# Kernel tuning notes

Hardware: AMD Instinct MI355X
Metric: run time of the kernel (lower is better)

The kernel has to match this reference:

```python
import jax, jax.numpy as jnp
import numpy as np

# Module config (from init_kwargs)
B = 1024          # batch
CIN = 1024        # in_channels
COUT = 2048       # out_channels
K = 7             # kernel_size; input spatial must equal K so deform-conv out is 1x1
STRIDE, PAD, DIL, DG = 1, 0, 1, 1  # stride, padding, dilation, deformable_groups
H = W = K


def setup_inputs() -> dict:
    key = jax.random.key(0)
    k1, k2, k3, k4, k5, k6 = jax.random.split(key, 6)
    x = jax.random.normal(k1, (B, CIN, H, W), dtype=jnp.float32)
    # offset-predicting conv: Conv2d(CIN, 2*K*K*DG, K, bias=False); small init so offsets are a few pixels
    offset_w = jax.random.normal(k2, (2 * DG * K * K, CIN, K, K), dtype=jnp.float32) * 0.01
    # deformable conv weight/bias (kaiming-like scale)
    deform_w = jax.random.normal(k3, (COUT, CIN, K, K), dtype=jnp.float32) * (1.0 / np.sqrt(CIN * K * K))
    deform_b = jax.random.normal(k4, (COUT,), dtype=jnp.float32) * 0.01
    # fused linear COUT -> COUT
    lin_w = jax.random.normal(k5, (COUT, COUT), dtype=jnp.float32) * (1.0 / np.sqrt(COUT))
    lin_b = jax.random.normal(k6, (COUT,), dtype=jnp.float32) * 0.01
    return {"x": x, "offset_w": offset_w, "deform_w": deform_w,
            "deform_b": deform_b, "lin_w": lin_w, "lin_b": lin_b}


def _deform_conv2d(x, offset, weight, bias):
    """torchvision deform_conv2d (v1, no modulation mask), groups=1.
    x: [B, C, H, W]; offset: [B, 2*DG*K*K, Ho, Wo] ordered (dg, kh, kw, (dy,dx)).
    """
    Bn, C, Hx, Wx = x.shape
    Cout, _, Kh, Kw = weight.shape
    P = Kh * Kw
    Ho, Wo = offset.shape[2], offset.shape[3]
    L = Ho * Wo
    Cg = C // DG

    off = offset.reshape(Bn, DG, P, 2, Ho, Wo)
    ky = jnp.repeat(jnp.arange(Kh), Kw).astype(x.dtype)   # [P]
    kx = jnp.tile(jnp.arange(Kw), Kh).astype(x.dtype)     # [P]
    base_y = (jnp.arange(Ho) * STRIDE - PAD).astype(x.dtype)  # [Ho]
    base_x = (jnp.arange(Wo) * STRIDE - PAD).astype(x.dtype)  # [Wo]
    # sampling positions [B, DG, P, Ho, Wo]
    py = off[:, :, :, 0] + (ky * DIL)[None, None, :, None, None] + base_y[None, None, None, :, None]
    px = off[:, :, :, 1] + (kx * DIL)[None, None, :, None, None] + base_x[None, None, None, None, :]

    y0 = jnp.floor(py); x0 = jnp.floor(px)
    fy = py - y0;       fx = px - x0
    y0i = y0.astype(jnp.int32); x0i = x0.astype(jnp.int32)

    xg = x.reshape(Bn, DG, Cg, Hx * Wx)
    acc = jnp.zeros((Bn, DG, Cg, P * L), x.dtype)
    for di, wy in ((0, 1.0 - fy), (1, fy)):
        for dj, wx in ((0, 1.0 - fx), (1, fx)):
            yi = y0i + di
            xi = x0i + dj
            valid = (yi >= 0) & (yi < Hx) & (xi >= 0) & (xi < Wx)  # zero-pad outside
            idx = (jnp.clip(yi, 0, Hx - 1) * Wx + jnp.clip(xi, 0, Wx - 1)).reshape(Bn, DG, 1, P * L)
            wgt = (wy * wx * valid.astype(x.dtype)).reshape(Bn, DG, 1, P * L)
            g = jnp.take_along_axis(xg, jnp.broadcast_to(idx, (Bn, DG, Cg, P * L)), axis=-1)
            acc = acc + g * wgt
    # columns: [B, C*P, L] with (channel, kernel-tap) ordering matching weight layout
    cols = acc.reshape(Bn, DG, Cg, P, L).reshape(Bn, C * P, L)
    out = jnp.einsum('ok,bkl->bol', weight.reshape(Cout, C * P), cols) + bias[None, :, None]
    return out.reshape(Bn, Cout, Ho, Wo)


def reference(x, offset_w, deform_w, deform_b, lin_w, lin_b):
    # 1) offset-predicting conv (bias=False)
    offset = jax.lax.conv_general_dilated(
        x, offset_w, window_strides=(STRIDE, STRIDE),
        padding=[(PAD, PAD), (PAD, PAD)], rhs_dilation=(DIL, DIL),
        dimension_numbers=('NCHW', 'OIHW', 'NCHW'))  # [B, 2*DG*K*K, 1, 1]
    # 2) deformable conv
    y = _deform_conv2d(x, offset, deform_w, deform_b)  # [B, COUT, 1, 1]
    # 3) linear over flattened features (spatial is 1x1 so flat dim == COUT)
    y = y.reshape(B, COUT) @ lin_w.T + lin_b
    # 4) softshrink(lambd=0.5)
    y = jnp.where(y > 0.5, y - 0.5, jnp.where(y < -0.5, y + 0.5, jnp.zeros_like(y)))
    return y.reshape(B, COUT, 1, 1)
```

## Files before the change

### kernel.cpp

```cpp
#include <hip/hip_runtime.h>

typedef _Float16 f16;
typedef _Float16 f16x8 __attribute__((ext_vector_type(8)));
typedef float f32x4 __attribute__((ext_vector_type(4)));

#define DEVI static __device__ __forceinline__

DEVI void async_ld16(const void* g, void* l) {
  __builtin_amdgcn_global_load_lds(
      (const __attribute__((address_space(1))) unsigned int*)g,
      (__attribute__((address_space(3))) unsigned int*)l, 16, 0, 0);
}

DEVI int sw_off(int row, int q) {
  return row * 64 + ((q ^ ((row >> 1) & 3)) << 4);
}

template<bool A_F32>
__global__ __launch_bounds__(256, 4)
void gemm_bt(const void* __restrict__ Aptr, const f16* __restrict__ Bt,
             float* __restrict__ Cpart, int ldK, int Nvalid,
             int mTiles, int nTiles, int kPerSplit, int Mtot) {
  __shared__ __align__(16) f16 As[128 * 32];
  __shared__ __align__(16) f16 Bs[128 * 32];

  int nb = gridDim.x;
  int bid = (blockIdx.x & 7) * (nb >> 3) + (blockIdx.x >> 3);
  int ms = bid % mTiles; bid /= mTiles;
  int ns = bid % nTiles; bid /= nTiles;
  int ks = bid;
  int m0 = ms * 128, n0 = ns * 128;
  int k0 = ks * kPerSplit;

  int tid = threadIdx.x;
  int w = tid >> 6, lane = tid & 63;
  int wrow = (w >> 1) * 64, wcol = (w & 1) * 64;
  int lrow = lane & 15, lquad = lane >> 4;

  f32x4 acc[4][4];
#pragma unroll
  for (int i = 0; i < 4; ++i)
#pragma unroll
    for (int j = 0; j < 4; ++j) acc[i][j] = (f32x4){0.f, 0.f, 0.f, 0.f};

  for (int kk = k0; kk < k0 + kPerSplit; kk += 32) {
    __syncthreads();
#pragma unroll
    for (int s = 0; s < 2; ++s) {
      int rl = w * 32 + s * 16 + (lane >> 2);
      int qp = lane & 3;
      int q = qp ^ ((rl >> 1) & 3);
      int rb = n0 + rl; if (rb > Nvalid - 1) rb = Nvalid - 1;
      async_ld16(Bt + (size_t)rb * ldK + kk + q * 8, &Bs[(w * 32 + s * 16) * 32]);
    }
    if (!A_F32) {
      const f16* Ah = (const f16*)Aptr;
#pragma unroll
      for (int s = 0; s < 2; ++s) {
        int rl = w * 32 + s * 16 + (lane >> 2);
        int qp = lane & 3;
        int q = qp ^ ((rl >> 1) & 3);
        async_ld16(Ah + (size_t)(m0 + rl) * ldK + kk + q * 8, &As[(w * 32 + s * 16) * 32]);
      }
    } else {
      const float* Af = (const float*)Aptr;
      int r = tid >> 1, half = tid & 1;
      const float* src = Af + (size_t)(m0 + r) * ldK + kk + half * 16;
#pragma unroll
      for (int u2 = 0; u2 < 2; ++u2) {
        f32x4 a = *(const f32x4*)(src + u2 * 8);
        f32x4 b = *(const f32x4*)(src + u2 * 8 + 4);
        f16x8 h;
        h[0] = (f16)a[0]; h[1] = (f16)a[1]; h[2] = (f16)a[2]; h[3] = (f16)a[3];
        h[4] = (f16)b[0]; h[5] = (f16)b[1]; h[6] = (f16)b[2]; h[7] = (f16)b[3];
        *(f16x8*)((char*)As + sw_off(r, half * 2 + u2)) = h;
      }
    }
    __syncthreads();

    f16x8 af[4], bf[4];
#pragma unroll
    for (int i = 0; i < 4; ++i)
      af[i] = *(const f16x8*)((const char*)As + sw_off(wrow + i * 16 + lrow, lquad));
#pragma unroll
    for (int j = 0; j < 4; ++j)
      bf[j] = *(const f16x8*)((const char*)Bs + sw_off(wcol + j * 16 + lrow, lquad));
#pragma unroll
    for (int i = 0; i < 4; ++i)
#pragma unroll
      for (int j = 0; j < 4; ++j)
        acc[i][j] = __builtin_amdgcn_mfma_f32_16x16x32_f16(af[i], bf[j], acc[i][j], 0, 0, 0);
  }

  size_t base = (size_t)ks * Mtot * Nvalid;
#pragma unroll
  for (int i = 0; i < 4; ++i) {
    int row = m0 + wrow + i * 16 + lquad * 4;
#pragma unroll
    for (int j = 0; j < 4; ++j) {
      int col = n0 + wcol + j * 16 + lrow;
      if (col < Nvalid) {
#pragma unroll
        for (int r = 0; r < 4; ++r)
          Cpart[base + (size_t)(row + r) * Nvalid + col] = acc[i][j][r];
      }
    }
  }
}

__global__ void cvt_f32_to_f16(const float* __restrict__ in, f16* __restrict__ out, long n) {
  long idx = ((long)blockIdx.x * blockDim.x + threadIdx.x) * 8;
  if (idx + 8 <= n) {
    f32x4 a = *(const f32x4*)(in + idx);
    f32x4 b = *(const f32x4*)(in + idx + 4);
    f16x8 o;
    o[0] = (f16)a[0]; o[1] = (f16)a[1]; o[2] = (f16)a[2]; o[3] = (f16)a[3];
    o[4] = (f16)b[0]; o[5] = (f16)b[1]; o[6] = (f16)b[2]; o[7] = (f16)b[3];
    *(f16x8*)(out + idx) = o;
  }
}

__global__ __launch_bounds__(256, 4)
void build_cols(const float* __restrict__ x, const float* __restrict__ offs,
                f16* __restrict__ cols) {
  int b = blockIdx.x >> 3;
  int c0 = (blockIdx.x & 7) * 128;
  __shared__ __align__(16) float s_x[128 * 49];
  __shared__ __align__(16) int   s_idx[49][4];
  __shared__ __align__(16) float s_w[49][4];
  int t = threadIdx.x;
  if (t < 49) {
    float dy = offs[b * 98 + 2 * t];
    float dx = offs[b * 98 + 2 * t + 1];
    float py = dy + (float)(t / 7);
    float px = dx + (float)(t % 7);
    float fy0 = floorf(py), fx0 = floorf(px);
    int y0 = (int)fy0, x0 = (int)fx0;
    float fy = py - fy0, fx = px - fx0;
#pragma unroll
    for (int di = 0; di < 2; ++di)
#pragma unroll
      for (int dj = 0; dj < 2; ++dj) {
        int yi = y0 + di, xi = x0 + dj;
        bool valid = (yi >= 0) && (yi < 7) && (xi >= 0) && (xi < 7);
        int yc = yi < 0 ? 0 : (yi > 6 ? 6 : yi);
        int xc = xi < 0 ? 0 : (xi > 6 ? 6 : xi);
        float wy = di ? fy : 1.f - fy;
        float wx = dj ? fx : 1.f - fx;
        s_idx[t][di * 2 + dj] = yc * 7 + xc;
        s_w[t][di * 2 + dj] = valid ? wy * wx : 0.f;
      }
  }
  const f32x4* xs = (const f32x4*)(x + (size_t)b * 50176 + c0 * 49);
  f32x4* s4 = (f32x4*)s_x;
#pragma unroll
  for (int i = 0; i < 6; ++i) s4[t + i * 256] = xs[t + i * 256];
  if (t < 32) s4[1536 + t] = xs[1536 + t];
  __syncthreads();

  f16* cb = cols + (size_t)b * 50176 + c0 * 49;
#pragma unroll
  for (int i = 0; i < 25; ++i) {
    int o = t + i * 256;
    if (o < 6272) {
      unsigned c = (unsigned)o / 49u;
      unsigned p = (unsigned)o - c * 49u;
      int4  gi = *(const int4*)s_idx[p];
      float4 gw = *(const float4*)s_w[p];
      const float* row = s_x + c * 49;
      float v = gw.x * row[gi.x] + gw.y * row[gi.y]
              + gw.z * row[gi.z] + gw.w * row[gi.w];
      cb[o] = (f16)v;
    }
  }
}

__global__ void combine_k(const float* __restrict__ parts, int nparts, size_t pstride,
                          const float* __restrict__ bias, float* __restrict__ outf,
                          f16* __restrict__ outh, int total, int cols, int shrink) {
  int i = blockIdx.x * 256 + threadIdx.x;
  if (i >= total) return;
  float s = 0.f;
  for (int p = 0; p < nparts; ++p) s += parts[(size_t)p * pstride + i];
  if (bias) s += bias[i % cols];
  if (shrink) s = s > 0.5f ? s - 0.5f : (s < -0.5f ? s + 0.5f : 0.f);
  if (outf) outf[i] = s;
  if (outh) outh[i] = (f16)s;
}

extern "C" void kernel_launch(void* const* d_in, const int* in_sizes, int n_in,
                              void* d_out, int out_size, void* d_ws, size_t ws_size,
                              hipStream_t stream) {
  const float* x  = (const float*)d_in[0];
  const float* ow = (const float*)d_in[1];
  const float* dw = (const float*)d_in[2];
  const float* db = (const float*)d_in[3];
  const float* lw = (const float*)d_in[4];
  const float* lb = (const float*)d_in[5];
  float* out = (float*)d_out;

  const long KX = 50176;
  char* ws = (char*)d_ws;
  size_t off = 0;
  auto alloc = [&](size_t bytes) {
    char* p = ws + off;
    off = (off + bytes + 255) & ~(size_t)255;
    return p;
  };
  f16*   dw_h = (f16*)  alloc((size_t)2048 * KX * 2);
  f16*   ow_h = (f16*)  alloc((size_t)98 * KX * 2);
  f16*   lw_h = (f16*)  alloc((size_t)2048 * 2048 * 2);
  f16*   cols = (f16*)  alloc((size_t)1024 * KX * 2);
  float* y1p  = (float*)alloc((size_t)8 * 1024 * 2048 * 4);
  f16*   y1h  = (f16*)  alloc((size_t)1024 * 2048 * 2);
  float* offs = (float*)y1p;
  float* offp = (float*)((char*)y1p + (1u << 20));
  float* y2p  = (float*)cols;
  if (off > ws_size) return;

  long n_dw = 2048L * KX, n_ow = 98L * KX, n_lw = 2048L * 2048L;
  cvt_f32_to_f16<<<(unsigned)(n_dw / 8 / 256), 256, 0, stream>>>(dw, dw_h, n_dw);
  cvt_f32_to_f16<<<(unsigned)(n_ow / 8 / 256), 256, 0, stream>>>(ow, ow_h, n_ow);
  cvt_f32_to_f16<<<(unsigned)(n_lw / 8 / 256), 256, 0, stream>>>(lw, lw_h, n_lw);

  gemm_bt<true><<<8 * 1 * 98, 256, 0, stream>>>(
      x, ow_h, offp, 50176, 98, 8, 1, 512, 1024);
  combine_k<<<(1024 * 98 + 255) / 256, 256, 0, stream>>>(
      offp, 98, (size_t)1024 * 98, nullptr, offs, nullptr, 1024 * 98, 98, 0);

  build_cols<<<1024 * 8, 256, 0, stream>>>(x, offs, cols);

  gemm_bt<false><<<8 * 16 * 8, 256, 0, stream>>>(
      cols, dw_h, y1p, 50176, 2048, 8, 16, 6272, 1024);
  combine_k<<<(2097152 + 255) / 256, 256, 0, stream>>>(
      y1p, 8, (size_t)2097152, db, nullptr, y1h, 2097152, 2048, 0);

  gemm_bt<false><<<8 * 16 * 8, 256, 0, stream>>>(
      y1h, lw_h, y2p, 2048, 2048, 8, 16, 256, 1024);
  combine_k<<<(2097152 + 255) / 256, 256, 0, stream>>>(
      y2p, 8, (size_t)2097152, lb, out, nullptr, 2097152, 2048, 1);
}
```

Measured before the change: 1.115 ms.

## Replace main deform GEMM with 256x256 double-buffered pipelined MFMA kernel

Result: faster. 1.032 ms (-7.4%).

```diff
diff --git a/kernel.cpp b/kernel.cpp
--- a/kernel.cpp
+++ b/kernel.cpp
@@ -107,6 +107,133 @@
     }
   }
 }
+
+#define DSR(dst, addr, off) \
+  asm volatile("ds_read_b128 %0, %1 offset:" off : "=&v"(dst) : "v"(addr))
+
+#define PHASE(BUF, KK, RH, RDB, STG, VMF, VMS, BAR) do {                      \
+    unsigned aP = aAddr + (unsigned)((BUF)*32768 + (KK)*16384 + (RH)*4096);   \
+    DSR(af[0], aP, "0");    DSR(af[1], aP, "1024");                           \
+    DSR(af[2], aP, "2048"); DSR(af[3], aP, "3072");                           \
+    if (RDB) {                                                                \
+      unsigned bP = bAddr + (unsigned)((BUF)*32768 + (KK)*16384);             \
+      DSR(bf[0], bP, "0");    DSR(bf[1], bP, "1024");                         \
+      DSR(bf[2], bP, "2048"); DSR(bf[3], bP, "3072");                         \
+    }                                                                         \
+    STG;                                                                      \
+    if (BAR) __builtin_amdgcn_s_barrier();                                    \
+    asm volatile("s_waitcnt lgkmcnt(0)");                                     \
+    __builtin_amdgcn_sched_barrier(0);                                        \
+    __builtin_amdgcn_s_setprio(1);                                            \
+    _Pragma("unroll")                                                         \
+    for (int i_ = 0; i_ < 4; ++i_) {                                          \
+      _Pragma("unroll")                                                       \
+      for (int j_ = 0; j_ < 4; ++j_)                                          \
+        acc[(RH)*4 + i_][j_] = __builtin_amdgcn_mfma_f32_16x16x32_f16(        \
+            af[i_], bf[j_], acc[(RH)*4 + i_][j_], 0, 0, 0);                   \
+    }                                                                         \
+    __builtin_amdgcn_s_setprio(0);                                            \
+    if (VMF) asm volatile("s_waitcnt vmcnt(" VMS ")");                        \
+    if (BAR) __builtin_amdgcn_s_barrier();                                    \
+  } while (0)
+
+__global__ __launch_bounds__(512, 2)
+void gemm256(const f16* __restrict__ A, const f16* __restrict__ Bt,
+             float* __restrict__ Cpart, int ldK,
+             int mTiles, int nTiles, int kPerSplit, int Mtot, int Ntot) {
+  __shared__ __align__(16) f16 lds[65536];
+
+  int nb = gridDim.x;
+  int bid = (blockIdx.x & 7) * (nb >> 3) + (blockIdx.x >> 3);
+  int ms = bid % mTiles; bid /= mTiles;
+  int ns = bid % nTiles; bid /= nTiles;
+  int ks = bid;
+  int m0 = ms * 256, n0 = ns * 256;
+  long k0 = (long)ks * kPerSplit;
+  int NT = kPerSplit >> 6;
+
+  int tid = threadIdx.x;
+  int w = tid >> 6, lane = tid & 63;
+  int wrow = (w >> 2) * 128, wcol = (w & 3) * 64;
+  int lrow = lane & 15;
+  unsigned sq = (unsigned)((((lane >> 4) ^ ((lrow >> 1) & 3))) << 4);
+
+  char* ldsc = (char*)&lds[0];
+  unsigned ldsBase = (unsigned)(uintptr_t)(void*)&lds[0];
+  unsigned aAddr = ldsBase + (unsigned)((wrow + lrow) * 64) + sq;
+  unsigned bAddr = ldsBase + 65536u + (unsigned)((wcol + lrow) * 64) + sq;
+
+  const f16* Ab = A + (size_t)m0 * ldK + k0;
+  const f16* Bb = Bt + (size_t)n0 * ldK + k0;
+  int rs = (w * 2) * 16 + (lane >> 2);
+  int qg = ((lane & 3) ^ ((rs >> 1) & 3)) * 8;
+  const f16* a0 = Ab + (size_t)rs * ldK + qg;
+  const f16* b0 = Bb + (size_t)rs * ldK + qg;
+  const f16* a1 = a0 + (size_t)16 * ldK;
+  const f16* b1 = b0 + (size_t)16 * ldK;
+
+#define STGP(p0, p1, LOFF, KOFF) do {                                \
+    async_ld16(p0 + (KOFF), ldsc + (LOFF) + (w * 2) * 1024);         \
+    async_ld16(p1 + (KOFF), ldsc + (LOFF) + (w * 2) * 1024 + 1024);  \
+  } while (0)
+#define STG_A(BUF, KK, KT) STGP(a0, a1, (BUF)*32768 + (KK)*16384, (KT)*64 + (KK)*32)
+#define STG_B(BUF, KK, KT) STGP(b0, b1, 65536 + (BUF)*32768 + (KK)*16384, (KT)*64 + (KK)*32)
+
+  f32x4 acc[8][4];
+#pragma unroll
+  for (int i = 0; i < 8; ++i)
+#pragma unroll
+    for (int j = 0; j < 4; ++j) acc[i][j] = (f32x4){0.f, 0.f, 0.f, 0.f};
+
+  f16x8 af[4], bf[4];
+
+  STG_B(0, 0, 0); STG_A(0, 0, 0);
+  STG_B(0, 1, 0); STG_A(0, 1, 0);
+  STG_B(1, 0, 1); STG_A(1, 0, 1);
+  asm volatile("s_waitcnt vmcnt(8)");
+  __builtin_amdgcn_s_barrier();
+
+  for (int t = 0; t + 3 < NT; t += 2) {
+    PHASE(0, 0, 0, 1, STG_B(1, 1, t + 1), 0, "0", 1);
+    PHASE(0, 0, 1, 0, STG_A(1, 1, t + 1), 1, "8", 1);
+    PHASE(0, 1, 0, 1, STG_B(0, 0, t + 2), 0, "0", 1);
+    PHASE(0, 1, 1, 0, STG_A(0, 0, t + 2), 1, "8", 1);
+    PHASE(1, 0, 0, 1, STG_B(0, 1, t + 2), 0, "0", 1);
+    PHASE(1, 0, 1, 0, STG_A(0, 1, t + 2), 1, "8", 1);
+    PHASE(1, 1, 0, 1, STG_B(1, 0, t + 3), 0, "0", 1);
+    PHASE(1, 1, 1, 0, STG_A(1, 0, t + 3), 1, "8", 1);
+  }
+
+  {
+    int km1 = NT - 1;
+    PHASE(0, 0, 0, 1, STG_B(1, 1, km1), 0, "0", 1);
+    PHASE(0, 0, 1, 0, STG_A(1, 1, km1), 1, "8", 1);
+    PHASE(0, 1, 0, 1, (void)0,          0, "0", 1);
+    PHASE(0, 1, 1, 0, (void)0,          1, "4", 1);
+    PHASE(1, 0, 0, 1, (void)0,          0, "0", 1);
+    PHASE(1, 0, 1, 0, (void)0,          1, "0", 1);
+    PHASE(1, 1, 0, 1, (void)0,          0, "0", 1);
+    PHASE(1, 1, 1, 0, (void)0,          0, "0", 0);
+  }
+
+  size_t cbase = (size_t)ks * ((size_t)Mtot * Ntot);
+#pragma unroll
+  for (int rt = 0; rt < 8; ++rt) {
+    int row = m0 + wrow + rt * 16 + (lane >> 4) * 4;
+#pragma unroll
+    for (int ct = 0; ct < 4; ++ct) {
+      int col = n0 + wcol + ct * 16 + lrow;
+#pragma unroll
+      for (int r = 0; r < 4; ++r)
+        Cpart[cbase + (size_t)(row + r) * Ntot + col] = acc[rt][ct][r];
+    }
+  }
+#undef STG_B
+#undef STG_A
+#undef STGP
+}
+#undef PHASE
+#undef DSR
 
 __global__ void cvt_f32_to_f16(const float* __restrict__ in, f16* __restrict__ out, long n) {
   long idx = ((long)blockIdx.x * blockDim.x + threadIdx.x) * 8;
@@ -230,8 +357,8 @@
 
   build_cols<<<1024 * 8, 256, 0, stream>>>(x, offs, cols);
 
-  gemm_bt<false><<<8 * 16 * 8, 256, 0, stream>>>(
-      cols, dw_h, y1p, 50176, 2048, 8, 16, 6272, 1024);
+  gemm256<<<256, 512, 0, stream>>>(
+      cols, dw_h, y1p, 50176, 4, 8, 6272, 1024, 2048);
   combine_k<<<(2097152 + 255) / 256, 256, 0, stream>>>(
       y1p, 8, (size_t)2097152, db, nullptr, y1h, 2097152, 2048, 0);
 
```
